# Kernel tuning notes

Measured on AMD Instinct MI355X. Metric: run time of the kernel, lower is better.

## Reference

```python
import jax, jax.numpy as jnp
import numpy as np

N, E, F_IN, H, F = 50000, 800000, 256, 2, 64
NEG_SLOPE = 0.2  # nn.LeakyReLU default in pytorch-GAT GATLayer


def gat_layer(x, edge_index, W, a_src, a_trg, Wskip, b, concat, act):
    n = x.shape[0]
    proj = (x @ W).reshape(n, H, F)                      # (N,H,F)
    s_src = (proj * a_src).sum(-1)                       # (N,H)
    s_trg = (proj * a_trg).sum(-1)                       # (N,H)
    src, trg = edge_index[0], edge_index[1]
    scores = jax.nn.leaky_relu(s_src[src] + s_trg[trg], NEG_SLOPE)  # (E,H)
    scores = scores - jax.lax.stop_gradient(scores.max())            # global max shift (as in source)
    exp = jnp.exp(scores)
    denom = jax.ops.segment_sum(exp, trg, num_segments=n)            # (N,H)
    att = (exp / (denom[trg] + 1e-16))[..., None]                    # (E,H,1)
    msgs = proj[src] * att                                           # (E,H,F) lifted+weighted
    out = jax.ops.segment_sum(msgs, trg, num_segments=n)             # (N,H,F)
    out = out + (x @ Wskip).reshape(n, H, F)                         # skip projection (dims differ)
    out = out.reshape(n, H * F) if concat else out.mean(axis=1)
    out = out + b
    return act(out)


def setup_inputs() -> dict:
    key = jax.random.key(0)
    ks = jax.random.split(key, 12)
    g = lambda k, shp, fan: jax.random.normal(k, shp, jnp.float32) / np.sqrt(fan)
    return {
        "x": jax.random.normal(ks[0], (N, F_IN), jnp.float32),
        "edge_index": jax.random.randint(ks[1], (2, E), 0, N),
        "W0": g(ks[2], (F_IN, H * F), F_IN),
        "a_src0": g(ks[3], (1, H, F), F),
        "a_trg0": g(ks[4], (1, H, F), F),
        "Wskip0": g(ks[5], (F_IN, H * F), F_IN),
        "b0": jnp.zeros((H * F,), jnp.float32),
        "W2": g(ks[6], (H * F, H * F), H * F),
        "a_src2": g(ks[7], (1, H, F), F),
        "a_trg2": g(ks[8], (1, H, F), F),
        "Wskip2": g(ks[9], (H * F, H * F), H * F),
        "b2": jnp.zeros((F,), jnp.float32),
    }


def reference(x, edge_index, W0, a_src0, a_trg0, Wskip0, b0, W2, a_src2, a_trg2, Wskip2, b2):
    h = gat_layer(x, edge_index, W0, a_src0, a_trg0, Wskip0, b0, True, jax.nn.elu)
    h = jax.nn.relu(h)  # HGGNN inter-layer ReLU (dropout is identity in eval)
    out = gat_layer(h, edge_index, W2, a_src2, a_trg2, Wskip2, b2, False, lambda z: z)
    return out
```

## Files before the change

kernel.cpp:

```cpp
#include <hip/hip_runtime.h>

#define NEG_SLOPE 0.2f
#define CBSH 7
#define MAXNC 512
#define BCAP 4096

typedef __attribute__((ext_vector_type(8))) short short8;
typedef __attribute__((ext_vector_type(4))) float f32x4;

__device__ __forceinline__ unsigned short f2bf(float f) {
  unsigned u = __float_as_uint(f);
  unsigned r = (u + 0x7FFFu + ((u >> 16) & 1u)) >> 16;
  return (unsigned short)r;
}
__device__ __forceinline__ unsigned pack_bf16(float lo, float hi) {
  return (unsigned)f2bf(lo) | ((unsigned)f2bf(hi) << 16);
}
__device__ __forceinline__ float bflo(unsigned u) {
  return __uint_as_float(u << 16);
}
__device__ __forceinline__ float bfhi(unsigned u) {
  return __uint_as_float(u & 0xFFFF0000u);
}
__device__ __forceinline__ void gload_lds16(const void* g, void* l) {
  __builtin_amdgcn_global_load_lds(
      (const __attribute__((address_space(1))) unsigned*)g,
      (__attribute__((address_space(3))) unsigned*)l, 16, 0, 0);
}

__global__ __launch_bounds__(256) void zerobuf(int* __restrict__ p, int n) {
  int i = blockIdx.x * 256 + threadIdx.x;
  if (i < n) p[i] = 0;
}

__global__ __launch_bounds__(256) void wconv(const float* __restrict__ W,
                                             unsigned* __restrict__ Wt, int K) {
  int per = K >> 3;
  int t = blockIdx.x * 256 + threadIdx.x;
  if (t >= 128 * per) return;
  int col = t / per;
  int kc = (t - col * per) << 3;
  float w[8];
#pragma unroll
  for (int j = 0; j < 8; ++j) w[j] = W[(size_t)(kc + j) * 128 + col];
  uint4 o = make_uint4(pack_bf16(w[0], w[1]), pack_bf16(w[2], w[3]),
                       pack_bf16(w[4], w[5]), pack_bf16(w[6], w[7]));
  *(uint4*)&Wt[((size_t)col * K + kc) >> 1] = o;
}

__global__ __launch_bounds__(256) void cscatter(const int* __restrict__ src,
                                                const int* __restrict__ trg,
                                                int* __restrict__ gcur,
                                                unsigned* __restrict__ EB,
                                                int E, int NC) {
  __shared__ int hist[MAXNC];
  __shared__ int gb[MAXNC];
  __shared__ int lcur[MAXNC];
  __shared__ unsigned lbuf[4096];
  __shared__ unsigned short cb16[4096];
  int tid = threadIdx.x;
  int e0 = blockIdx.x * 4096;
  int cnt = E - e0;
  if (cnt > 4096) cnt = 4096;
  for (int i = tid; i < NC; i += 256) hist[i] = 0;
  __syncthreads();
  unsigned pk[16];
  unsigned short cbr[16];
  int mine = 0;
#pragma unroll
  for (int j = 0; j < 16; ++j) {
    int i = tid + j * 256;
    if (i < cnt) {
      int e = e0 + i;
      int s = src[e];
      int t = trg[e];
      int cb = t >> CBSH;
      pk[j] = ((unsigned)s << CBSH) | (unsigned)(t & ((1 << CBSH) - 1));
      cbr[j] = (unsigned short)cb;
      atomicAdd(&hist[cb], 1);
      mine = j + 1;
    }
  }
  __syncthreads();
  for (int i = tid; i < NC; i += 256)
    gb[i] = hist[i] ? (i * BCAP + atomicAdd(&gcur[i], hist[i])) : 0;
  __syncthreads();
  if (tid == 0) {
    int run = 0;
    for (int i = 0; i < NC; ++i) {
      int v = hist[i];
      hist[i] = run;
      run += v;
    }
  }
  __syncthreads();
  for (int i = tid; i < NC; i += 256) lcur[i] = hist[i];
  __syncthreads();
  for (int j = 0; j < mine; ++j) {
    int p = atomicAdd(&lcur[cbr[j]], 1);
    lbuf[p] = pk[j];
    cb16[p] = cbr[j];
  }
  __syncthreads();
  for (int i = tid; i < cnt; i += 256) {
    int cb = cb16[i];
    EB[gb[cb] + (i - hist[cb])] = lbuf[i];
  }
}

__global__ __launch_bounds__(256) void bfill(const unsigned* __restrict__ EB,
                                             const int* __restrict__ gcur,
                                             int* __restrict__ rowbeg,
                                             int* __restrict__ rowend,
                                             int* __restrict__ SS, int N) {
  __shared__ int deg[128], lofs[128], cur[128];
  int cb = blockIdx.x;
  int b0 = cb * BCAP;
  int b1 = b0 + gcur[cb];
  int n0 = cb << CBSH;
  int tid = threadIdx.x;
  if (tid < 128) deg[tid] = 0;
  __syncthreads();
  for (int i = b0 + tid; i < b1; i += 256)
    atomicAdd(&deg[EB[i] & ((1 << CBSH) - 1)], 1);
  __syncthreads();
  if (tid == 0) {
    int run = b0;
    for (int l = 0; l < 128; ++l) {
      lofs[l] = run;
      run += deg[l];
    }
  }
  __syncthreads();
  if (tid < 128) {
    cur[tid] = lofs[tid];
    int n = n0 + tid;
    if (n < N) {
      rowbeg[n] = lofs[tid];
      rowend[n] = lofs[tid] + deg[tid];
    }
  }
  __syncthreads();
  for (int i = b0 + tid; i < b1; i += 256) {
    unsigned pk = EB[i];
    int pos = atomicAdd(&cur[pk & ((1 << CBSH) - 1)], 1);
    SS[pos] = (int)(pk >> CBSH);
  }
}

template <int KK, bool AF32>
__global__ __launch_bounds__(512) void gemm_dual(
    const void* __restrict__ Av, const unsigned* __restrict__ BtP,
    const unsigned* __restrict__ BtS, unsigned* __restrict__ Cb,
    unsigned* __restrict__ PH, const float* __restrict__ a_src,
    const float* __restrict__ a_trg, float* __restrict__ ssrc,
    float* __restrict__ strg, int M) {
  constexpr int NSTEP = KK / 32;
  __shared__ __align__(16) char ldsraw[33792];
  float(*Cs)[132] = (float(*)[132])ldsraw;

  const int tid = threadIdx.x;
  const int lane = tid & 63;
  const int w = tid >> 6;
  const int row0 = blockIdx.x * 128;

  f32x4 accP[8], accS[8];
#pragma unroll
  for (int c = 0; c < 8; ++c) {
    accP[c] = (f32x4)0.f;
    accS[c] = (f32x4)0.f;
  }

  const int arow = tid >> 2;
  const int akq = (tid & 3) << 3;
  const int agr = row0 + arow;
  const int abyte =
      ((((arow >> 4) << 6) | ((tid & 3) << 4) | (arow & 15)) << 4);
  const unsigned short* BP16 = (const unsigned short*)BtP;
  const unsigned short* BS16 = (const unsigned short*)BtS;
  const int bg = lane >> 4;
  const int br = lane & 15;

  for (int t = 0; t < NSTEP; ++t) {
    const int k0 = t << 5;
    {
      size_t eoff = (size_t)(16 * w + br) * KK + k0 + 8 * bg;
      gload_lds16(BP16 + eoff, ldsraw + 8192 + w * 1024);
      gload_lds16(BS16 + eoff, ldsraw + 16384 + w * 1024);
    }
    {
      uint4 p;
      if constexpr (AF32) {
        const float* A = (const float*)Av;
        float4 v0 = make_float4(0.f, 0.f, 0.f, 0.f), v1 = v0;
        if (agr < M) {
          v0 = *(const float4*)&A[(size_t)agr * KK + k0 + akq];
          v1 = *(const float4*)&A[(size_t)agr * KK + k0 + akq + 4];
        }
        p = make_uint4(pack_bf16(v0.x, v0.y), pack_bf16(v0.z, v0.w),
                       pack_bf16(v1.x, v1.y), pack_bf16(v1.z, v1.w));
      } else {
        const unsigned short* A = (const unsigned short*)Av;
        p = make_uint4(0u, 0u, 0u, 0u);
        if (agr < M) p = *(const uint4*)&A[(size_t)agr * KK + k0 + akq];
      }
      *(uint4*)(ldsraw + abyte) = p;
    }
    __syncthreads();
    short8 af = *(const short8*)(ldsraw + w * 1024 + lane * 16);
#pragma unroll
    for (int c = 0; c < 8; ++c) {
      short8 bp = *(const short8*)(ldsraw + 8192 + c * 1024 + lane * 16);
      accP[c] =
          __builtin_amdgcn_mfma_f32_16x16x32_bf16(af, bp, accP[c], 0, 0, 0);
      short8 bs = *(const short8*)(ldsraw + 16384 + c * 1024 + lane * 16);
      accS[c] =
          __builtin_amdgcn_mfma_f32_16x16x32_bf16(af, bs, accS[c], 0, 0, 0);
    }
    __syncthreads();
  }

  const int hrow = lane >> 5;
  const int c32 = lane & 31;
  const int wh = w >> 2;
  const int w4 = w & 3;

#pragma unroll
  for (int h = 0; h < 2; ++h) {
    if (wh == h) {
#pragma unroll
      for (int c = 0; c < 8; ++c)
#pragma unroll
        for (int r = 0; r < 4; ++r)
          Cs[16 * w4 + ((lane >> 4) << 2) + r][16 * c + (lane & 15)] =
              accP[c][r];
    }
    __syncthreads();
    if (wh == h) {
#pragma unroll
      for (int i = 0; i < 8; ++i) {
        int lr = 16 * w4 + 2 * i + hrow;
        int gr = row0 + 64 * h + lr;
        if (gr < M) {
          float4 v = *(const float4*)&Cs[lr][c32 * 4];
          *(uint2*)&PH[(size_t)gr * 64 + c32 * 2] =
              make_uint2(pack_bf16(v.x, v.y), pack_bf16(v.z, v.w));
        }
      }
      int tid4 = tid - h * 256;
      int srow = tid4 >> 2;
      int q = tid4 & 3;
      int gr = row0 + 64 * h + srow;
      float ds = 0.f, dt = 0.f;
#pragma unroll
      for (int j = 0; j < 8; ++j) {
        int col = q * 32 + j * 4;
        float4 v = *(const float4*)&Cs[srow][col];
        float4 asv = *(const float4*)&a_src[col];
        float4 atv = *(const float4*)&a_trg[col];
        ds += v.x * asv.x + v.y * asv.y + v.z * asv.z + v.w * asv.w;
        dt += v.x * atv.x + v.y * atv.y + v.z * atv.z + v.w * atv.w;
      }
      ds += __shfl_xor(ds, 1, 64);
      dt += __shfl_xor(dt, 1, 64);
      if (gr < M && (q & 1) == 0) {
        int hh = q >> 1;
        ssrc[gr * 2 + hh] = ds;
        strg[gr * 2 + hh] = dt;
      }
    }
    __syncthreads();
  }

#pragma unroll
  for (int h = 0; h < 2; ++h) {
    if (wh == h) {
#pragma unroll
      for (int c = 0; c < 8; ++c)
#pragma unroll
        for (int r = 0; r < 4; ++r)
          Cs[16 * w4 + ((lane >> 4) << 2) + r][16 * c + (lane & 15)] =
              accS[c][r];
    }
    __syncthreads();
    if (wh == h) {
#pragma unroll
      for (int i = 0; i < 8; ++i) {
        int lr = 16 * w4 + 2 * i + hrow;
        int gr = row0 + 64 * h + lr;
        if (gr < M) {
          float4 v = *(const float4*)&Cs[lr][c32 * 4];
          *(uint2*)&Cb[(size_t)gr * 64 + c32 * 2] =
              make_uint2(pack_bf16(v.x, v.y), pack_bf16(v.z, v.w));
        }
      }
    }
    __syncthreads();
  }
}

template <int LAYER>
__global__ __launch_bounds__(256) void aggregate(
    const int* __restrict__ rowbeg, const int* __restrict__ rowend,
    const int* __restrict__ SS, const float2* __restrict__ ssrc,
    const float2* __restrict__ strg, const unsigned* __restrict__ PH,
    const unsigned* __restrict__ Sb, const float* __restrict__ bias,
    void* __restrict__ Outv, int Nn) {
  int wid = (int)((blockIdx.x * blockDim.x + threadIdx.x) >> 6);
  int lane = threadIdx.x & 63;
  if (wid >= Nn) return;
  int n = wid;
  bool hi = lane >= 32;
  float2 st2 = strg[n];
  float stv = hi ? st2.y : st2.x;
  int beg = rowbeg[n];
  int end = rowend[n];
  float accx = 0.f, accy = 0.f, dsum = 0.f;

  for (int base = beg; base < end; base += 32) {
    int cnt = end - base;
    if (cnt > 32) cnt = 32;
    int ej = lane & 31;
    int idx = base + ej;
    bool valid = idx < end;
    int sv = valid ? SS[idx] : 0;
    float2 es = ssrc[sv];
    float z = (hi ? es.y : es.x) + stv;
    z = (z >= 0.f) ? z : NEG_SLOPE * z;
    float g = __expf(z);
    if (!valid) g = 0.f;
    {
      float gr = g;
#pragma unroll
      for (int m = 1; m < 32; m <<= 1) gr += __shfl_xor(gr, m, 64);
      dsum += gr;
    }
    int j = 0;
    for (; j + 8 <= cnt; j += 8) {
      unsigned wv[8];
      float gh[8];
#pragma unroll
      for (int k = 0; k < 8; ++k) {
        int s = __builtin_amdgcn_readlane(sv, j + k);
        wv[k] = PH[(size_t)s * 64 + lane];
      }
#pragma unroll
      for (int k = 0; k < 8; ++k) gh[k] = __shfl(g, j + k, 32);
#pragma unroll
      for (int k = 0; k < 8; ++k) {
        accx = fmaf(bflo(wv[k]), gh[k], accx);
        accy = fmaf(bfhi(wv[k]), gh[k], accy);
      }
    }
    for (; j < cnt; ++j) {
      int s = __builtin_amdgcn_readlane(sv, j);
      unsigned wv = PH[(size_t)s * 64 + lane];
      float gh = __shfl(g, j, 32);
      accx = fmaf(bflo(wv), gh, accx);
      accy = fmaf(bfhi(wv), gh, accy);
    }
  }

  float inv = 1.0f / (dsum + 1e-16f);
  accx *= inv;
  accy *= inv;
  unsigned skv = Sb[(size_t)n * 64 + lane];
  float skx = bflo(skv);
  float sky = bfhi(skv);
  if (LAYER == 1) {
    float2 b = *(const float2*)&bias[lane * 2];
    float zx = fmaxf(accx + skx + b.x, 0.f);
    float zy = fmaxf(accy + sky + b.y, 0.f);
    ((unsigned*)Outv)[(size_t)n * 64 + lane] = pack_bf16(zx, zy);
  } else {
    float zx = accx + skx;
    float zy = accy + sky;
    float ox = __shfl(zx, lane + 32, 64);
    float oy = __shfl(zy, lane + 32, 64);
    if (lane < 32) {
      float2 b = *(const float2*)&bias[lane * 2];
      float rx = 0.5f * (zx + ox) + b.x;
      float ry = 0.5f * (zy + oy) + b.y;
      *(float2*)&((float*)Outv)[(size_t)n * 64 + lane * 2] =
          make_float2(rx, ry);
    }
  }
}

extern "C" void kernel_launch(void* const* d_in, const int* in_sizes, int n_in,
                              void* d_out, int out_size, void* d_ws,
                              size_t ws_size, hipStream_t stream) {
  const float* x = (const float*)d_in[0];
  const int* ei = (const int*)d_in[1];
  const float* W0 = (const float*)d_in[2];
  const float* a_src0 = (const float*)d_in[3];
  const float* a_trg0 = (const float*)d_in[4];
  const float* Wsk0 = (const float*)d_in[5];
  const float* b0 = (const float*)d_in[6];
  const float* W2 = (const float*)d_in[7];
  const float* a_src2 = (const float*)d_in[8];
  const float* a_trg2 = (const float*)d_in[9];
  const float* Wsk2 = (const float*)d_in[10];
  const float* b2 = (const float*)d_in[11];

  const int FIN = 256;
  const int N = in_sizes[0] / FIN;
  const int E = in_sizes[1] / 2;
  const int* src = ei;
  const int* trg = ei + E;
  const int NC = (N + (1 << CBSH) - 1) >> CBSH;

  char* base = (char*)d_ws;
  size_t off = 0;
  auto alloc = [&](size_t bytes) -> void* {
    void* p = base + off;
    off += (bytes + 255) & ~(size_t)255;
    return p;
  };
  unsigned* PH = (unsigned*)alloc((size_t)N * 64 * sizeof(unsigned));
  unsigned* Sb = (unsigned*)alloc((size_t)N * 64 * sizeof(unsigned));
  unsigned* Hb = (unsigned*)alloc((size_t)N * 64 * sizeof(unsigned));
  int* SS = (int*)alloc((size_t)NC * BCAP * sizeof(int));
  unsigned* EB = (unsigned*)alloc((size_t)NC * BCAP * sizeof(unsigned));
  float* ssrc = (float*)alloc((size_t)N * 2 * sizeof(float));
  float* strg = (float*)alloc((size_t)N * 2 * sizeof(float));
  int* rowbeg = (int*)alloc((size_t)N * sizeof(int));
  int* rowend = (int*)alloc((size_t)N * sizeof(int));
  int* gcur = (int*)alloc((size_t)MAXNC * sizeof(int));
  unsigned* WtP0 = (unsigned*)alloc((size_t)128 * 256 * 2);
  unsigned* WtS0 = (unsigned*)alloc((size_t)128 * 256 * 2);
  unsigned* WtP2 = (unsigned*)alloc((size_t)128 * 128 * 2);
  unsigned* WtS2 = (unsigned*)alloc((size_t)128 * 128 * 2);

  dim3 blk(256);
  dim3 blk512(512);
  int gemmBlocks = (N + 127) / 128;
  int nodeBlocks = (N + 3) / 4;
  int chunkBlocks = (E + 4095) / 4096;

  zerobuf<<<2, blk, 0, stream>>>(gcur, MAXNC);

  wconv<<<16, blk, 0, stream>>>(W0, WtP0, 256);
  wconv<<<16, blk, 0, stream>>>(Wsk0, WtS0, 256);
  wconv<<<8, blk, 0, stream>>>(W2, WtP2, 128);
  wconv<<<8, blk, 0, stream>>>(Wsk2, WtS2, 128);

  cscatter<<<chunkBlocks, blk, 0, stream>>>(src, trg, gcur, EB, E, NC);
  bfill<<<NC, blk, 0, stream>>>(EB, gcur, rowbeg, rowend, SS, N);

  gemm_dual<256, true><<<gemmBlocks, blk512, 0, stream>>>(
      x, WtP0, WtS0, Sb, PH, a_src0, a_trg0, ssrc, strg, N);
  aggregate<1><<<nodeBlocks, blk, 0, stream>>>(
      rowbeg, rowend, SS, (const float2*)ssrc, (const float2*)strg, PH, Sb, b0,
      Hb, N);
  gemm_dual<128, false><<<gemmBlocks, blk512, 0, stream>>>(
      Hb, WtP2, WtS2, Sb, PH, a_src2, a_trg2, ssrc, strg, N);
  aggregate<2><<<nodeBlocks, blk, 0, stream>>>(
      rowbeg, rowend, SS, (const float2*)ssrc, (const float2*)strg, PH, Sb, b2,
      d_out, N);
}
```

Measured before the change: 169.0 us.

## Merge weight prep kernels and co-schedule edge scatter with layer-1 GEMM

Replaces the zerobuf and four wconv launches with one prep kernel. The edge-bucket scatter now shares a launch with the first-layer GEMM through a block-index split, so the two independent stages run side by side. The scatter is reworked for 512-thread blocks and reuses the GEMM's LDS buffer, which cuts launch count and fills idle CUs during the GEMM. The cost is that scatter blocks now carry the GEMM's 512-thread launch bounds and LDS footprint, which can lower occupancy for both paths.

```diff
diff --git a/kernel.cpp b/kernel.cpp
--- a/kernel.cpp
+++ b/kernel.cpp
@@ -28,16 +28,10 @@
       (__attribute__((address_space(3))) unsigned*)l, 16, 0, 0);
 }
 
-__global__ __launch_bounds__(256) void zerobuf(int* __restrict__ p, int n) {
-  int i = blockIdx.x * 256 + threadIdx.x;
-  if (i < n) p[i] = 0;
-}
-
-__global__ __launch_bounds__(256) void wconv(const float* __restrict__ W,
-                                             unsigned* __restrict__ Wt, int K) {
+__device__ __forceinline__ void wconv_item(const float* __restrict__ W,
+                                           unsigned* __restrict__ Wt, int K,
+                                           int t) {
   int per = K >> 3;
-  int t = blockIdx.x * 256 + threadIdx.x;
-  if (t >= 128 * per) return;
   int col = t / per;
   int kc = (t - col * per) << 3;
   float w[8];
@@ -48,28 +42,42 @@
   *(uint4*)&Wt[((size_t)col * K + kc) >> 1] = o;
 }
 
-__global__ __launch_bounds__(256) void cscatter(const int* __restrict__ src,
-                                                const int* __restrict__ trg,
-                                                int* __restrict__ gcur,
-                                                unsigned* __restrict__ EB,
-                                                int E, int NC) {
-  __shared__ int hist[MAXNC];
-  __shared__ int gb[MAXNC];
-  __shared__ int lcur[MAXNC];
-  __shared__ unsigned lbuf[4096];
-  __shared__ unsigned short cb16[4096];
+__global__ __launch_bounds__(256) void prep(
+    const float* __restrict__ W0, const float* __restrict__ Ws0,
+    const float* __restrict__ W2c, const float* __restrict__ Ws2,
+    unsigned* __restrict__ WtP0, unsigned* __restrict__ WtS0,
+    unsigned* __restrict__ WtP2, unsigned* __restrict__ WtS2,
+    int* __restrict__ gcur) {
+  int t = blockIdx.x * 256 + threadIdx.x;
+  if (t < 4096) wconv_item(W0, WtP0, 256, t);
+  else if (t < 8192) wconv_item(Ws0, WtS0, 256, t - 4096);
+  else if (t < 10240) wconv_item(W2c, WtP2, 128, t - 8192);
+  else if (t < 12288) wconv_item(Ws2, WtS2, 128, t - 10240);
+  else if (t < 12288 + MAXNC) gcur[t - 12288] = 0;
+}
+
+__device__ void cscatter_body(char* ldsraw, int chunk,
+                              const int* __restrict__ src,
+                              const int* __restrict__ trg,
+                              int* __restrict__ gcur,
+                              unsigned* __restrict__ EB, int E, int NC) {
+  int* hist = (int*)ldsraw;
+  int* gb = hist + MAXNC;
+  int* lcur = gb + MAXNC;
+  unsigned* lbuf = (unsigned*)(lcur + MAXNC);
+  unsigned short* cb16 = (unsigned short*)(lbuf + 4096);
   int tid = threadIdx.x;
-  int e0 = blockIdx.x * 4096;
+  int e0 = chunk * 4096;
   int cnt = E - e0;
   if (cnt > 4096) cnt = 4096;
-  for (int i = tid; i < NC; i += 256) hist[i] = 0;
-  __syncthreads();
-  unsigned pk[16];
-  unsigned short cbr[16];
+  for (int i = tid; i < NC; i += 512) hist[i] = 0;
+  __syncthreads();
+  unsigned pk[8];
+  unsigned short cbr[8];
   int mine = 0;
 #pragma unroll
-  for (int j = 0; j < 16; ++j) {
-    int i = tid + j * 256;
+  for (int j = 0; j < 8; ++j) {
+    int i = tid + j * 512;
     if (i < cnt) {
       int e = e0 + i;
       int s = src[e];
@@ -82,7 +90,7 @@
     }
   }
   __syncthreads();
-  for (int i = tid; i < NC; i += 256)
+  for (int i = tid; i < NC; i += 512)
     gb[i] = hist[i] ? (i * BCAP + atomicAdd(&gcur[i], hist[i])) : 0;
   __syncthreads();
   if (tid == 0) {
@@ -94,7 +102,7 @@
     }
   }
   __syncthreads();
-  for (int i = tid; i < NC; i += 256) lcur[i] = hist[i];
+  for (int i = tid; i < NC; i += 512) lcur[i] = hist[i];
   __syncthreads();
   for (int j = 0; j < mine; ++j) {
     int p = atomicAdd(&lcur[cbr[j]], 1);
@@ -102,7 +110,7 @@
     cb16[p] = cbr[j];
   }
   __syncthreads();
-  for (int i = tid; i < cnt; i += 256) {
+  for (int i = tid; i < cnt; i += 512) {
     int cb = cb16[i];
     EB[gb[cb] + (i - hist[cb])] = lbuf[i];
   }
@@ -149,20 +157,21 @@
 }
 
 template <int KK, bool AF32>
-__global__ __launch_bounds__(512) void gemm_dual(
-    const void* __restrict__ Av, const unsigned* __restrict__ BtP,
-    const unsigned* __restrict__ BtS, unsigned* __restrict__ Cb,
-    unsigned* __restrict__ PH, const float* __restrict__ a_src,
-    const float* __restrict__ a_trg, float* __restrict__ ssrc,
-    float* __restrict__ strg, int M) {
+__device__ void gemm_body(char* ldsraw, int row0, const void* __restrict__ Av,
+                          const unsigned* __restrict__ BtP,
+                          const unsigned* __restrict__ BtS,
+                          unsigned* __restrict__ Cb,
+                          unsigned* __restrict__ PH,
+                          const float* __restrict__ a_src,
+                          const float* __restrict__ a_trg,
+                          float* __restrict__ ssrc, float* __restrict__ strg,
+                          int M) {
   constexpr int NSTEP = KK / 32;
-  __shared__ __align__(16) char ldsraw[33792];
   float(*Cs)[132] = (float(*)[132])ldsraw;
 
   const int tid = threadIdx.x;
   const int lane = tid & 63;
   const int w = tid >> 6;
-  const int row0 = blockIdx.x * 128;
 
   f32x4 accP[8], accS[8];
 #pragma unroll
@@ -297,6 +306,34 @@
     }
     __syncthreads();
   }
+}
+
+__global__ __launch_bounds__(512) void fused1(
+    const float* __restrict__ x, const unsigned* __restrict__ WtP0,
+    const unsigned* __restrict__ WtS0, unsigned* __restrict__ Sb,
+    unsigned* __restrict__ PH, const float* __restrict__ a_src0,
+    const float* __restrict__ a_trg0, float* __restrict__ ssrc,
+    float* __restrict__ strg, int M, int GB, const int* __restrict__ src,
+    const int* __restrict__ trg, int* __restrict__ gcur,
+    unsigned* __restrict__ EB, int E, int NC) {
+  __shared__ __align__(16) char ldsraw[33792];
+  if ((int)blockIdx.x < GB) {
+    gemm_body<256, true>(ldsraw, blockIdx.x * 128, x, WtP0, WtS0, Sb, PH,
+                         a_src0, a_trg0, ssrc, strg, M);
+  } else {
+    cscatter_body(ldsraw, blockIdx.x - GB, src, trg, gcur, EB, E, NC);
+  }
+}
+
+__global__ __launch_bounds__(512) void gemm2(
+    const void* __restrict__ Hb, const unsigned* __restrict__ WtP2,
+    const unsigned* __restrict__ WtS2, unsigned* __restrict__ Sb,
+    unsigned* __restrict__ PH, const float* __restrict__ a_src2,
+    const float* __restrict__ a_trg2, float* __restrict__ ssrc,
+    float* __restrict__ strg, int M) {
+  __shared__ __align__(16) char ldsraw[33792];
+  gemm_body<128, false>(ldsraw, blockIdx.x * 128, Hb, WtP2, WtS2, Sb, PH,
+                        a_src2, a_trg2, ssrc, strg, M);
 }
 
 template <int LAYER>
@@ -437,24 +474,21 @@
   int gemmBlocks = (N + 127) / 128;
   int nodeBlocks = (N + 3) / 4;
   int chunkBlocks = (E + 4095) / 4096;
-
-  zerobuf<<<2, blk, 0, stream>>>(gcur, MAXNC);
-
-  wconv<<<16, blk, 0, stream>>>(W0, WtP0, 256);
-  wconv<<<16, blk, 0, stream>>>(Wsk0, WtS0, 256);
-  wconv<<<8, blk, 0, stream>>>(W2, WtP2, 128);
-  wconv<<<8, blk, 0, stream>>>(Wsk2, WtS2, 128);
-
-  cscatter<<<chunkBlocks, blk, 0, stream>>>(src, trg, gcur, EB, E, NC);
+  int prepBlocks = (12288 + MAXNC + 255) / 256;
+
+  prep<<<prepBlocks, blk, 0, stream>>>(W0, Wsk0, W2, Wsk2, WtP0, WtS0, WtP2,
+                                       WtS2, gcur);
+
+  fused1<<<gemmBlocks + chunkBlocks, blk512, 0, stream>>>(
+      x, WtP0, WtS0, Sb, PH, a_src0, a_trg0, ssrc, strg, N, gemmBlocks, src,
+      trg, gcur, EB, E, NC);
   bfill<<<NC, blk, 0, stream>>>(EB, gcur, rowbeg, rowend, SS, N);
 
-  gemm_dual<256, true><<<gemmBlocks, blk512, 0, stream>>>(
-      x, WtP0, WtS0, Sb, PH, a_src0, a_trg0, ssrc, strg, N);
   aggregate<1><<<nodeBlocks, blk, 0, stream>>>(
       rowbeg, rowend, SS, (const float2*)ssrc, (const float2*)strg, PH, Sb, b0,
       Hb, N);
-  gemm_dual<128, false><<<gemmBlocks, blk512, 0, stream>>>(
-      Hb, WtP2, WtS2, Sb, PH, a_src2, a_trg2, ssrc, strg, N);
+  gemm2<<<gemmBlocks, blk512, 0, stream>>>(Hb, WtP2, WtS2, Sb, PH, a_src2,
+                                           a_trg2, ssrc, strg, N);
   aggregate<2><<<nodeBlocks, blk, 0, stream>>>(
       rowbeg, rowend, SS, (const float2*)ssrc, (const float2*)strg, PH, Sb, b2,
       d_out, N);
```

Result: faster. 143.7 us (-15.0%).
